# Kernel optimization log

Measured on AMD Instinct MI355X. Metric: run time of the kernel, lower is better.

Reference implementation:

```python
import jax, jax.numpy as jnp
from jax import lax
import numpy as np

EPS = 1e-5
TOPK_RATIO = 0.6

def _bn(y, gamma, beta, mean, var):
    # inference-mode BatchNorm3d over channel axis 1
    scale = gamma / jnp.sqrt(var + EPS)
    return (y - mean[None, :, None, None, None]) * scale[None, :, None, None, None] + beta[None, :, None, None, None]

def setup_inputs() -> dict:
    key = jax.random.key(0)
    ks = jax.random.split(key, 8)
    B, C, D, H, W = 4, 64, 16, 64, 64
    C8 = max(4, C // 8)  # bottleneck channels = 8
    x = jax.random.normal(ks[0], (B, C, D, H, W), dtype=jnp.float32)
    # depthwise conv weight, OIDHW with I=1 (groups=C), kernel (1,5,5)
    w_dw = jax.random.normal(ks[1], (C, 1, 1, 5, 5), dtype=jnp.float32) * 0.05
    bn1_gamma = jnp.ones((C,), jnp.float32)
    bn1_beta = jnp.zeros((C,), jnp.float32)
    bn1_mean = jax.random.normal(ks[2], (C,), jnp.float32) * 0.1
    bn1_var = jax.random.uniform(ks[3], (C,), jnp.float32, 0.5, 1.5)
    # pointwise 1x1x1 convs as matrices
    w_pw1 = jax.random.normal(ks[4], (C8, C), jnp.float32) * 0.05
    b_pw1 = jnp.zeros((C8,), jnp.float32)
    bn2_gamma = jnp.ones((C8,), jnp.float32)
    bn2_beta = jnp.zeros((C8,), jnp.float32)
    bn2_mean = jax.random.normal(ks[5], (C8,), jnp.float32) * 0.1
    bn2_var = jax.random.uniform(ks[6], (C8,), jnp.float32, 0.5, 1.5)
    w_pw2 = jax.random.normal(ks[7], (C, C8), jnp.float32) * 0.05
    b_pw2 = jnp.zeros((C,), jnp.float32)
    alpha = jnp.ones((), jnp.float32)
    return {"x": x, "w_dw": w_dw,
            "bn1_gamma": bn1_gamma, "bn1_beta": bn1_beta, "bn1_mean": bn1_mean, "bn1_var": bn1_var,
            "w_pw1": w_pw1, "b_pw1": b_pw1,
            "bn2_gamma": bn2_gamma, "bn2_beta": bn2_beta, "bn2_mean": bn2_mean, "bn2_var": bn2_var,
            "w_pw2": w_pw2, "b_pw2": b_pw2, "alpha": alpha}

def reference(x, w_dw, bn1_gamma, bn1_beta, bn1_mean, bn1_var,
              w_pw1, b_pw1, bn2_gamma, bn2_beta, bn2_mean, bn2_var,
              w_pw2, b_pw2, alpha):
    B, C, D, H, W = x.shape
    # branch1: depthwise conv3d (1,5,5), pad (0,2,2) + BN + SiLU
    y1 = lax.conv_general_dilated(
        x, w_dw, window_strides=(1, 1, 1),
        padding=((0, 0), (2, 2), (2, 2)),
        dimension_numbers=("NCDHW", "OIDHW", "NCDHW"),
        feature_group_count=C)
    y1 = jax.nn.silu(_bn(y1, bn1_gamma, bn1_beta, bn1_mean, bn1_var))
    # branch2: 1x1 conv -> BN -> SiLU -> 1x1 conv
    y2 = jnp.einsum("oc,bcdhw->bodhw", w_pw1, x) + b_pw1[None, :, None, None, None]
    y2 = jax.nn.silu(_bn(y2, bn2_gamma, bn2_beta, bn2_mean, bn2_var))
    y2 = jnp.einsum("oc,bcdhw->bodhw", w_pw2, y2) + b_pw2[None, :, None, None, None]
    attn = y1 * y2
    # channel-wise top-k threshold per spatial location
    k = max(1, int(TOPK_RATIO * C))
    attn_cl = jnp.moveaxis(attn, 1, -1)  # (B,D,H,W,C)
    thr = lax.top_k(attn_cl, k)[0][..., -1]  # k-th largest, (B,D,H,W)
    mask = (attn >= thr[:, None, :, :, :]).astype(attn.dtype)
    return x + alpha * (attn * mask)
```

## Files before the change

### kernel.cpp

```cpp
#include <hip/hip_runtime.h>

#define B  4
#define C  64
#define C8 8
#define DD 16
#define H  64
#define W  64
#define EPSV 1e-5f

__global__ __launch_bounds__(256) void dwconv_kernel(
    const float* __restrict__ x, const float* __restrict__ w_dw,
    const float* __restrict__ g1, const float* __restrict__ be1,
    const float* __restrict__ mu1, const float* __restrict__ va1,
    float* __restrict__ y1)
{
    const int blk = blockIdx.x;
    const int half = threadIdx.x >> 7;
    const int t = threadIdx.x & 127;
    const int cpair = blk & 31;
    const int d = (blk >> 5) & 15;
    const int b = blk >> 9;
    const int c = cpair * 2 + half;

    float wk[25];
#pragma unroll
    for (int i = 0; i < 25; ++i) wk[i] = w_dw[c * 25 + i];
    const float scale = g1[c] * rsqrtf(va1[c] + EPSV);
    const float shift = be1[c] - mu1[c] * scale;

    const int w8 = (t & 7) * 8;
    const int h4 = (t >> 3) * 4;
    const long base = ((long)(b * C + c) * DD + d) * (H * W);

    float acc[4][8];
#pragma unroll
    for (int i = 0; i < 4; ++i)
#pragma unroll
        for (int ow = 0; ow < 8; ++ow) acc[i][ow] = 0.f;

#pragma unroll
    for (int j = 0; j < 8; ++j) {
        const int r = h4 + j - 2;
        if (r >= 0 && r < H) {
            const float4* rowp = (const float4*)(x + base + r * W);
            const int q = w8 >> 2;
            const float4 z = make_float4(0.f, 0.f, 0.f, 0.f);
            float4 v0 = (w8 > 0)  ? rowp[q - 1] : z;
            float4 v1 = rowp[q];
            float4 v2 = rowp[q + 1];
            float4 v3 = (w8 < 56) ? rowp[q + 2] : z;
            float vals[16] = {v0.x, v0.y, v0.z, v0.w,
                              v1.x, v1.y, v1.z, v1.w,
                              v2.x, v2.y, v2.z, v2.w,
                              v3.x, v3.y, v3.z, v3.w};
#pragma unroll
            for (int i = 0; i < 4; ++i) {
                if (i <= j && (j - i) <= 4) {
                    const int kr = j - i;
#pragma unroll
                    for (int dw = 0; dw < 5; ++dw) {
                        const float kw = wk[kr * 5 + dw];
#pragma unroll
                        for (int ow = 0; ow < 8; ++ow)
                            acc[i][ow] += kw * vals[ow + dw + 2];
                    }
                }
            }
        }
    }

#pragma unroll
    for (int i = 0; i < 4; ++i) {
        const int h = h4 + i;
        float o[8];
#pragma unroll
        for (int ow = 0; ow < 8; ++ow) {
            const float v = acc[i][ow] * scale + shift;
            o[ow] = v * (1.f / (1.f + __expf(-v)));
        }
        *(float4*)(y1 + base + h * W + w8)     = make_float4(o[0], o[1], o[2], o[3]);
        *(float4*)(y1 + base + h * W + w8 + 4) = make_float4(o[4], o[5], o[6], o[7]);
    }
}

__global__ __launch_bounds__(256) void fuse_kernel(
    const float* __restrict__ x, const float* __restrict__ y1,
    const float* __restrict__ w1, const float* __restrict__ b1,
    const float* __restrict__ g2, const float* __restrict__ be2,
    const float* __restrict__ mu2, const float* __restrict__ va2,
    const float* __restrict__ w2, const float* __restrict__ b2,
    const float* __restrict__ alphap, float* __restrict__ out)
{
    const int gid = blockIdx.x * 256 + threadIdx.x;
    const int b = gid >> 16;
    const int r = gid & 65535;
    const long base = (long)b * (C * 65536) + r;

    float s1[C8];
#pragma unroll
    for (int o = 0; o < C8; ++o) s1[o] = 0.f;
#pragma unroll
    for (int c = 0; c < C; ++c) {
        const float xc = x[base + (long)c * 65536];
#pragma unroll
        for (int o = 0; o < C8; ++o) s1[o] += w1[o * C + c] * xc;
    }
    float hh[C8];
#pragma unroll
    for (int o = 0; o < C8; ++o) {
        const float sc = g2[o] * rsqrtf(va2[o] + EPSV);
        const float v = (s1[o] + b1[o] - mu2[o]) * sc + be2[o];
        hh[o] = v * (1.f / (1.f + __expf(-v)));
    }

    float t[C];
#pragma unroll
    for (int c = 0; c < C; ++c) {
        float y2 = b2[c];
#pragma unroll
        for (int o = 0; o < C8; ++o) y2 += w2[c * C8 + o] * hh[o];
        t[c] = y1[base + (long)c * 65536] * y2;
    }

#pragma unroll
    for (int k = 2; k <= 64; k <<= 1) {
#pragma unroll
        for (int j = k >> 1; j > 0; j >>= 1) {
#pragma unroll
            for (int i = 0; i < 64; ++i) {
                const int l = i ^ j;
                if (l > i) {
                    const float u = t[i], v = t[l];
                    const float mn = fminf(u, v), mx = fmaxf(u, v);
                    if ((i & k) == 0) { t[i] = mn; t[l] = mx; }
                    else              { t[i] = mx; t[l] = mn; }
                }
            }
        }
    }
    const float thr = t[26];
    const float alpha = alphap[0];

#pragma unroll
    for (int c = 0; c < C; ++c) {
        float y2 = b2[c];
#pragma unroll
        for (int o = 0; o < C8; ++o) y2 += w2[c * C8 + o] * hh[o];
        const float av = y1[base + (long)c * 65536] * y2;
        const float xc = x[base + (long)c * 65536];
        out[base + (long)c * 65536] = xc + ((av >= thr) ? alpha * av : 0.f);
    }
}

extern "C" void kernel_launch(void* const* d_in, const int* in_sizes, int n_in,
                              void* d_out, int out_size, void* d_ws, size_t ws_size,
                              hipStream_t stream) {
    const float* x    = (const float*)d_in[0];
    const float* w_dw = (const float*)d_in[1];
    const float* g1   = (const float*)d_in[2];
    const float* be1  = (const float*)d_in[3];
    const float* mu1  = (const float*)d_in[4];
    const float* va1  = (const float*)d_in[5];
    const float* w1   = (const float*)d_in[6];
    const float* b1   = (const float*)d_in[7];
    const float* g2   = (const float*)d_in[8];
    const float* be2  = (const float*)d_in[9];
    const float* mu2  = (const float*)d_in[10];
    const float* va2  = (const float*)d_in[11];
    const float* w2   = (const float*)d_in[12];
    const float* b2   = (const float*)d_in[13];
    const float* alp  = (const float*)d_in[14];
    float* out = (float*)d_out;
    float* y1  = (float*)d_ws;

    dwconv_kernel<<<(B * DD * C) / 2, 256, 0, stream>>>(x, w_dw, g1, be1, mu1, va1, y1);
    fuse_kernel<<<(B * DD * H * W) / 256, 256, 0, stream>>>(
        x, y1, w1, b1, g2, be2, mu2, va2, w2, b2, alp, out);
}
```

Baseline: 237.8 us.

## Store depthwise output channels-last and precompute bottleneck activations in separate kernel

The depthwise conv kernel now writes y1 in a channels-last layout (64 channels contiguous per spatial location), so the fuse kernel can read each location's channel vector with float4 loads. A new kernel computes the bottleneck SiLU activations into workspace when there is enough space, which takes the 64-channel x reduction out of the register-heavy sort kernel. The depthwise kernel's block mapping changes to 512 threads covering all channels for an 8-row strip. The risks are that the channels-last writes are strided scalar stores, the extra kernel adds traffic, and x is still read twice.

New measurement: 317.2 us. +33.4%, slower.

```diff
diff --git a/kernel.cpp b/kernel.cpp
--- a/kernel.cpp
+++ b/kernel.cpp
@@ -8,19 +8,62 @@
 #define W  64
 #define EPSV 1e-5f
 
-__global__ __launch_bounds__(256) void dwconv_kernel(
+__device__ __forceinline__ float silu_f(float v) {
+    return v * (1.f / (1.f + __expf(-v)));
+}
+
+__global__ __launch_bounds__(256) void pw_hh_kernel(
+    const float* __restrict__ x,
+    const float* __restrict__ w1, const float* __restrict__ b1,
+    const float* __restrict__ g2, const float* __restrict__ be2,
+    const float* __restrict__ mu2, const float* __restrict__ va2,
+    float* __restrict__ hht)
+{
+    const int gid = blockIdx.x * 256 + threadIdx.x;
+    const int loc = gid * 2;
+    const int b = loc >> 16;
+    const int r = loc & 65535;
+    const float* xp = x + (long)b * (C * 65536) + r;
+
+    float s0[C8], s1[C8];
+#pragma unroll
+    for (int o = 0; o < C8; ++o) { s0[o] = 0.f; s1[o] = 0.f; }
+#pragma unroll
+    for (int c = 0; c < C; ++c) {
+        const float2 xv = *(const float2*)(xp + (long)c * 65536);
+#pragma unroll
+        for (int o = 0; o < C8; ++o) {
+            const float wv = w1[o * C + c];
+            s0[o] += wv * xv.x;
+            s1[o] += wv * xv.y;
+        }
+    }
+    float out0[C8], out1[C8];
+#pragma unroll
+    for (int o = 0; o < C8; ++o) {
+        const float sc = g2[o] * rsqrtf(va2[o] + EPSV);
+        out0[o] = silu_f((s0[o] + b1[o] - mu2[o]) * sc + be2[o]);
+        out1[o] = silu_f((s1[o] + b1[o] - mu2[o]) * sc + be2[o]);
+    }
+    float4* op = (float4*)(hht + (long)loc * 8);
+    op[0] = make_float4(out0[0], out0[1], out0[2], out0[3]);
+    op[1] = make_float4(out0[4], out0[5], out0[6], out0[7]);
+    op[2] = make_float4(out1[0], out1[1], out1[2], out1[3]);
+    op[3] = make_float4(out1[4], out1[5], out1[6], out1[7]);
+}
+
+__global__ __launch_bounds__(512) void dwconv_kernel(
     const float* __restrict__ x, const float* __restrict__ w_dw,
     const float* __restrict__ g1, const float* __restrict__ be1,
     const float* __restrict__ mu1, const float* __restrict__ va1,
-    float* __restrict__ y1)
+    float* __restrict__ y1t)
 {
     const int blk = blockIdx.x;
-    const int half = threadIdx.x >> 7;
-    const int t = threadIdx.x & 127;
-    const int cpair = blk & 31;
-    const int d = (blk >> 5) & 15;
-    const int b = blk >> 9;
-    const int c = cpair * 2 + half;
+    const int hb = blk & 7;
+    const int d = (blk >> 3) & 15;
+    const int b = blk >> 7;
+    const int c  = threadIdx.x >> 3;
+    const int w8 = (threadIdx.x & 7) * 8;
 
     float wk[25];
 #pragma unroll
@@ -28,63 +71,63 @@
     const float scale = g1[c] * rsqrtf(va1[c] + EPSV);
     const float shift = be1[c] - mu1[c] * scale;
 
-    const int w8 = (t & 7) * 8;
-    const int h4 = (t >> 3) * 4;
-    const long base = ((long)(b * C + c) * DD + d) * (H * W);
-
-    float acc[4][8];
-#pragma unroll
-    for (int i = 0; i < 4; ++i)
-#pragma unroll
-        for (int ow = 0; ow < 8; ++ow) acc[i][ow] = 0.f;
-
-#pragma unroll
-    for (int j = 0; j < 8; ++j) {
-        const int r = h4 + j - 2;
-        if (r >= 0 && r < H) {
-            const float4* rowp = (const float4*)(x + base + r * W);
-            const int q = w8 >> 2;
-            const float4 z = make_float4(0.f, 0.f, 0.f, 0.f);
-            float4 v0 = (w8 > 0)  ? rowp[q - 1] : z;
-            float4 v1 = rowp[q];
-            float4 v2 = rowp[q + 1];
-            float4 v3 = (w8 < 56) ? rowp[q + 2] : z;
-            float vals[16] = {v0.x, v0.y, v0.z, v0.w,
-                              v1.x, v1.y, v1.z, v1.w,
-                              v2.x, v2.y, v2.z, v2.w,
-                              v3.x, v3.y, v3.z, v3.w};
-#pragma unroll
-            for (int i = 0; i < 4; ++i) {
-                if (i <= j && (j - i) <= 4) {
-                    const int kr = j - i;
-#pragma unroll
-                    for (int dw = 0; dw < 5; ++dw) {
-                        const float kw = wk[kr * 5 + dw];
-#pragma unroll
-                        for (int ow = 0; ow < 8; ++ow)
-                            acc[i][ow] += kw * vals[ow + dw + 2];
+    const long xbase = ((long)(b * C + c) * DD + d) * (H * W);
+    const int  bd    = (b * DD + d) * (H * W);
+    const int  hbase = hb * 8;
+    const int  q     = w8 >> 2;
+
+#pragma unroll
+    for (int g = 0; g < 2; ++g) {
+        float acc[4][8];
+#pragma unroll
+        for (int i = 0; i < 4; ++i)
+#pragma unroll
+            for (int ow = 0; ow < 8; ++ow) acc[i][ow] = 0.f;
+
+#pragma unroll
+        for (int j = 0; j < 8; ++j) {
+            const int r = hbase + g * 4 + j - 2;
+            if (r >= 0 && r < H) {
+                const float4* rowp = (const float4*)(x + xbase + r * W);
+                const float4 z = make_float4(0.f, 0.f, 0.f, 0.f);
+                float4 v0 = (w8 > 0)  ? rowp[q - 1] : z;
+                float4 v1 = rowp[q];
+                float4 v2 = rowp[q + 1];
+                float4 v3 = (w8 < 56) ? rowp[q + 2] : z;
+                float vals[16] = {v0.x, v0.y, v0.z, v0.w,
+                                  v1.x, v1.y, v1.z, v1.w,
+                                  v2.x, v2.y, v2.z, v2.w,
+                                  v3.x, v3.y, v3.z, v3.w};
+#pragma unroll
+                for (int i = 0; i < 4; ++i) {
+                    if (i <= j && (j - i) <= 4) {
+                        const int kr = j - i;
+#pragma unroll
+                        for (int dw = 0; dw < 5; ++dw) {
+                            const float kw = wk[kr * 5 + dw];
+#pragma unroll
+                            for (int ow = 0; ow < 8; ++ow)
+                                acc[i][ow] += kw * vals[ow + dw + 2];
+                        }
                     }
                 }
             }
         }
-    }
-
-#pragma unroll
-    for (int i = 0; i < 4; ++i) {
-        const int h = h4 + i;
-        float o[8];
-#pragma unroll
-        for (int ow = 0; ow < 8; ++ow) {
-            const float v = acc[i][ow] * scale + shift;
-            o[ow] = v * (1.f / (1.f + __expf(-v)));
-        }
-        *(float4*)(y1 + base + h * W + w8)     = make_float4(o[0], o[1], o[2], o[3]);
-        *(float4*)(y1 + base + h * W + w8 + 4) = make_float4(o[4], o[5], o[6], o[7]);
-    }
-}
-
+#pragma unroll
+        for (int i = 0; i < 4; ++i) {
+            const int h = hbase + g * 4 + i;
+            float* dst = y1t + ((long)(bd + h * W + w8)) * 64 + c;
+#pragma unroll
+            for (int ow = 0; ow < 8; ++ow)
+                dst[ow * 64] = silu_f(acc[i][ow] * scale + shift);
+        }
+    }
+}
+
+template<int HAVE_HH>
 __global__ __launch_bounds__(256) void fuse_kernel(
-    const float* __restrict__ x, const float* __restrict__ y1,
+    const float* __restrict__ x, const float* __restrict__ y1t,
+    const float* __restrict__ hht,
     const float* __restrict__ w1, const float* __restrict__ b1,
     const float* __restrict__ g2, const float* __restrict__ be2,
     const float* __restrict__ mu2, const float* __restrict__ va2,
@@ -94,32 +137,45 @@
     const int gid = blockIdx.x * 256 + threadIdx.x;
     const int b = gid >> 16;
     const int r = gid & 65535;
-    const long base = (long)b * (C * 65536) + r;
-
-    float s1[C8];
-#pragma unroll
-    for (int o = 0; o < C8; ++o) s1[o] = 0.f;
-#pragma unroll
-    for (int c = 0; c < C; ++c) {
-        const float xc = x[base + (long)c * 65536];
-#pragma unroll
-        for (int o = 0; o < C8; ++o) s1[o] += w1[o * C + c] * xc;
-    }
+    const float* xp = x + (long)b * (C * 65536) + r;
+    const float* y1p = y1t + (long)gid * 64;
+
     float hh[C8];
-#pragma unroll
-    for (int o = 0; o < C8; ++o) {
-        const float sc = g2[o] * rsqrtf(va2[o] + EPSV);
-        const float v = (s1[o] + b1[o] - mu2[o]) * sc + be2[o];
-        hh[o] = v * (1.f / (1.f + __expf(-v)));
+    if (HAVE_HH) {
+        const float4* hp = (const float4*)(hht + (long)gid * 8);
+        const float4 h0 = hp[0], h1 = hp[1];
+        hh[0] = h0.x; hh[1] = h0.y; hh[2] = h0.z; hh[3] = h0.w;
+        hh[4] = h1.x; hh[5] = h1.y; hh[6] = h1.z; hh[7] = h1.w;
+    } else {
+        float s1[C8];
+#pragma unroll
+        for (int o = 0; o < C8; ++o) s1[o] = 0.f;
+#pragma unroll
+        for (int c = 0; c < C; ++c) {
+            const float xc = xp[(long)c * 65536];
+#pragma unroll
+            for (int o = 0; o < C8; ++o) s1[o] += w1[o * C + c] * xc;
+        }
+#pragma unroll
+        for (int o = 0; o < C8; ++o) {
+            const float sc = g2[o] * rsqrtf(va2[o] + EPSV);
+            hh[o] = silu_f((s1[o] + b1[o] - mu2[o]) * sc + be2[o]);
+        }
     }
 
     float t[C];
 #pragma unroll
-    for (int c = 0; c < C; ++c) {
-        float y2 = b2[c];
-#pragma unroll
-        for (int o = 0; o < C8; ++o) y2 += w2[c * C8 + o] * hh[o];
-        t[c] = y1[base + (long)c * 65536] * y2;
+    for (int q4 = 0; q4 < 16; ++q4) {
+        const float4 yv = ((const float4*)y1p)[q4];
+        const float yy[4] = {yv.x, yv.y, yv.z, yv.w};
+#pragma unroll
+        for (int s = 0; s < 4; ++s) {
+            const int c = q4 * 4 + s;
+            float y2 = b2[c];
+#pragma unroll
+            for (int o = 0; o < C8; ++o) y2 += w2[c * C8 + o] * hh[o];
+            t[c] = yy[s] * y2;
+        }
     }
 
 #pragma unroll
@@ -140,15 +196,22 @@
     }
     const float thr = t[26];
     const float alpha = alphap[0];
-
-#pragma unroll
-    for (int c = 0; c < C; ++c) {
-        float y2 = b2[c];
-#pragma unroll
-        for (int o = 0; o < C8; ++o) y2 += w2[c * C8 + o] * hh[o];
-        const float av = y1[base + (long)c * 65536] * y2;
-        const float xc = x[base + (long)c * 65536];
-        out[base + (long)c * 65536] = xc + ((av >= thr) ? alpha * av : 0.f);
+    float* op = out + (long)b * (C * 65536) + r;
+
+#pragma unroll
+    for (int q4 = 0; q4 < 16; ++q4) {
+        const float4 yv = ((const float4*)y1p)[q4];
+        const float yy[4] = {yv.x, yv.y, yv.z, yv.w};
+#pragma unroll
+        for (int s = 0; s < 4; ++s) {
+            const int c = q4 * 4 + s;
+            float y2 = b2[c];
+#pragma unroll
+            for (int o = 0; o < C8; ++o) y2 += w2[c * C8 + o] * hh[o];
+            const float av = yy[s] * y2;
+            const float xc = xp[(long)c * 65536];
+            op[(long)c * 65536] = xc + ((av >= thr) ? alpha * av : 0.f);
+        }
     }
 }
 
@@ -171,9 +234,21 @@
     const float* b2   = (const float*)d_in[13];
     const float* alp  = (const float*)d_in[14];
     float* out = (float*)d_out;
-    float* y1  = (float*)d_ws;
-
-    dwconv_kernel<<<(B * DD * C) / 2, 256, 0, stream>>>(x, w_dw, g1, be1, mu1, va1, y1);
-    fuse_kernel<<<(B * DD * H * W) / 256, 256, 0, stream>>>(
-        x, y1, w1, b1, g2, be2, mu2, va2, w2, b2, alp, out);
-}
+
+    const size_t y1_bytes = (size_t)B * C * DD * H * W * 4;
+    const size_t hh_bytes = (size_t)B * C8 * DD * H * W * 4;
+    float* y1t = (float*)d_ws;
+    float* hht = (float*)((char*)d_ws + y1_bytes);
+    const bool have_hh = ws_size >= y1_bytes + hh_bytes;
+
+    dwconv_kernel<<<B * DD * 8, 512, 0, stream>>>(x, w_dw, g1, be1, mu1, va1, y1t);
+    if (have_hh) {
+        pw_hh_kernel<<<(B * DD * H * W) / 512, 256, 0, stream>>>(
+            x, w1, b1, g2, be2, mu2, va2, hht);
+        fuse_kernel<1><<<(B * DD * H * W) / 256, 256, 0, stream>>>(
+            x, y1t, hht, w1, b1, g2, be2, mu2, va2, w2, b2, alp, out);
+    } else {
+        fuse_kernel<0><<<(B * DD * H * W) / 256, 256, 0, stream>>>(
+            x, y1t, hht, w1, b1, g2, be2, mu2, va2, w2, b2, alp, out);
+    }
+}
```
